# Optimization experiments

Measured on AMD Instinct MI355X. Metric: run time of the kernel, lower is better.

## Reference

```python
import jax, jax.numpy as jnp
import numpy as np

GROUP_SIZE = 128
EQN = "btd,kdf->btkf"  # x:[B,T,D] @ w:[K,D,F] -> [B,T,K,F]


def setup_inputs() -> dict:
    key = jax.random.key(0)
    k1, k2, k3, k4 = jax.random.split(key, 4)
    B, T, D = 4, 2048, 4096
    K, F = 2, 8192
    G = D // GROUP_SIZE  # 32 quantization groups along D
    x = jax.random.normal(k1, (B, T, D), dtype=jnp.float32)
    qweight = jax.random.randint(k2, (K, D, F), 0, 16, dtype=jnp.int32)  # uint4 values
    qzeros = jax.random.randint(k3, (K, G, F), 0, 16, dtype=jnp.int32)   # uint4 zero points
    scales = jax.random.uniform(k4, (K, G, F), dtype=jnp.float32) * 0.02
    return {"x": x, "qweight": qweight, "qzeros": qzeros, "scales": scales}


def dequantize(imatrix, scales, zeros, group_size, axis_to_repeat):
    rs = jnp.repeat(scales, group_size, axis=axis_to_repeat)
    rz = jnp.repeat(zeros, group_size, axis=axis_to_repeat)
    return (imatrix.astype(rs.dtype) - rz.astype(rs.dtype)) * rs


def reference(x, qweight, qzeros, scales):
    # dequantize int4 weights along axis 1 (hidden/contraction dim), then einsum
    w = dequantize(qweight, scales, qzeros, GROUP_SIZE, axis_to_repeat=1)  # [K,D,F] fp32
    w = w.astype(x.dtype)
    return jnp.einsum(EQN, x, w)  # [B,T,K,F]
```

## Files before the change

kernel.cpp:

```cpp
#include <hip/hip_runtime.h>
#include <hip/hip_bf16.h>
#include <stdint.h>


typedef __attribute__((ext_vector_type(8))) short bf16x8;
typedef __attribute__((ext_vector_type(16))) float f32x16;
typedef __attribute__((ext_vector_type(4))) float f32x4;

static constexpr int Dd = 4096, Ff = 8192;
static constexpr int M = 8192, NTOT = 16384;
static constexpr int NKT2 = Dd / 32;
static constexpr int NMB = M / 256;
static constexpr int NNB = NTOT / 256;

__device__ __forceinline__ short f2bf(float f) {
    __hip_bfloat16 h = __float2bfloat16(f);
    return *reinterpret_cast<short*>(&h);
}

__device__ __forceinline__ int frag_off32(int r, int cb) {
    const int rb = r >> 5, ks = cb >> 1, kh = cb & 1;
    return ((rb * 2 + ks) << 10) + (((r & 31) + 32 * kh) << 4);
}

__global__ __launch_bounds__(256) void xcvt(const float* __restrict__ x,
                                            char* __restrict__ Xw) {
    const int bid = blockIdx.x;
    const int h = bid >> 7, kt2 = bid & 127;
    const int t = threadIdx.x;
    const int r = t >> 1, seg = t & 1;
    const float* src = x + ((size_t)(h * 128 + r)) * Dd + kt2 * 32 + seg * 16;
    char* panel = Xw + ((size_t)bid << 13);
    #pragma unroll
    for (int jj = 0; jj < 2; ++jj) {
        float4 v0 = *reinterpret_cast<const float4*>(src + jj * 8);
        float4 v1 = *reinterpret_cast<const float4*>(src + jj * 8 + 4);
        union { short s[8]; bf16x8 v; } u;
        u.s[0] = f2bf(v0.x); u.s[1] = f2bf(v0.y); u.s[2] = f2bf(v0.z); u.s[3] = f2bf(v0.w);
        u.s[4] = f2bf(v1.x); u.s[5] = f2bf(v1.y); u.s[6] = f2bf(v1.z); u.s[7] = f2bf(v1.w);
        const int cb = seg * 2 + jj;
        *reinterpret_cast<bf16x8*>(panel + frag_off32(r, cb)) = u.v;
    }
}

__global__ __launch_bounds__(256) void wdq(const int* __restrict__ qw,
                                           const int* __restrict__ qz,
                                           const float* __restrict__ sc,
                                           char* __restrict__ Ww) {
    const int bid = blockIdx.x;
    const int fh = bid >> 7, kt2 = bid & 127;
    const int t = threadIdx.x;
    const int r = t & 127, dh = t >> 7;
    const int n = fh * 128 + r;
    const int k = n >> 13, f = n & 8191;
    const int g = kt2 >> 2;
    const int   zv = qz[((size_t)k * 32 + g) * Ff + f];
    const float sv = sc[((size_t)k * 32 + g) * Ff + f];
    const int* qp = qw + ((size_t)(k * Dd + kt2 * 32 + dh * 16)) * Ff + f;
    char* panel = Ww + ((size_t)bid << 13);
    #pragma unroll
    for (int jj = 0; jj < 2; ++jj) {
        union { short s[8]; bf16x8 v; } u;
        #pragma unroll
        for (int e = 0; e < 8; ++e) {
            int q = qp[(size_t)(jj * 8 + e) * Ff];
            u.s[e] = f2bf((float)(q - zv) * sv);
        }
        const int cb = dh * 2 + jj;
        *reinterpret_cast<bf16x8*>(panel + frag_off32(r, cb)) = u.v;
    }
}

#define APAN32(H, KT2) (Xw + (((size_t)(H) * 128 + (KT2)) << 13))
#define BPAN32(H, KT2) (Ww + (((size_t)(H) * 128 + (KT2)) << 13))

#define GLL(GP, LP)                                                                \
    __builtin_amdgcn_global_load_lds(                                              \
        (const __attribute__((address_space(1))) void*)(GP),                       \
        (__attribute__((address_space(3))) void*)(LP), 16, 0, 0)

#define STAGE_TILE(KT2, BUF) do {                                                  \
    GLL(APAN32(bm2,     (KT2)) + woff16, (BUF) +     0 + woffu);                   \
    GLL(APAN32(bm2 + 1, (KT2)) + woff16, (BUF) +  8192 + woffu);                   \
    GLL(BPAN32(bn2,     (KT2)) + woff16, (BUF) + 16384 + woffu);                   \
    GLL(BPAN32(bn2 + 1, (KT2)) + woff16, (BUF) + 24576 + woffu);                   \
} while (0)

#define SB0() __builtin_amdgcn_sched_barrier(0)

#define BODY(KT2, BUFR, DOST, BUFS) do {                                           \
    if (DOST) STAGE_TILE((KT2) + 2, BUFS);                                         \
    bf16x8 a[8], b[4];                                                             \
    _Pragma("unroll")                                                              \
    for (int mb = 0; mb < 4; ++mb)                                                 \
        _Pragma("unroll")                                                          \
        for (int ks = 0; ks < 2; ++ks)                                             \
            a[mb * 2 + ks] = *reinterpret_cast<const bf16x8*>(                     \
                (BUFR) + aoff + (mb * 2 + ks) * 1024);                             \
    _Pragma("unroll")                                                              \
    for (int nf = 0; nf < 2; ++nf)                                                 \
        _Pragma("unroll")                                                          \
        for (int ks = 0; ks < 2; ++ks)                                             \
            b[nf * 2 + ks] = *reinterpret_cast<const bf16x8*>(                     \
                (BUFR) + boff + nf * 2048 + ks * 1024);                            \
    _Pragma("unroll")                                                              \
    for (int ks = 0; ks < 2; ++ks)                                                 \
        _Pragma("unroll")                                                          \
        for (int mb = 0; mb < 4; ++mb)                                             \
            _Pragma("unroll")                                                      \
            for (int nf = 0; nf < 2; ++nf)                                         \
                acc[mb * 2 + nf] = __builtin_amdgcn_mfma_f32_32x32x16_bf16(        \
                    a[mb * 2 + ks], b[nf * 2 + ks], acc[mb * 2 + nf], 0, 0, 0);    \
    if (DOST) asm volatile("s_waitcnt vmcnt(4)" ::: "memory");                     \
    else      asm volatile("s_waitcnt vmcnt(0)" ::: "memory");                     \
    SB0();                                                                         \
    __builtin_amdgcn_s_barrier();                                                  \
    SB0();                                                                         \
} while (0)

__global__ __launch_bounds__(512, 2) void gemm256(const char* __restrict__ Xw,
                                                  const char* __restrict__ Ww,
                                                  float* __restrict__ out) {
    __shared__ char lds[131072];
    char* const L0 = lds;
    char* const L1 = lds + 32768;
    char* const L2 = lds + 65536;
    char* const L3 = lds + 98304;

    const int t = threadIdx.x;
    const int wave = t >> 6, lane = t & 63;
    const int wm = wave >> 2, wn = wave & 3;
    const int l31 = lane & 31;
    const int lane16 = lane << 4;

    const int xcd = blockIdx.x & 7;
    const int c   = blockIdx.x >> 3;
    const int bn  = xcd * 8 + (c >> 5);
    const int bm  = c & 31;
    const int bm2 = bm * 2, bn2 = bn * 2;

    const int woff16 = wave * 1024 + lane16;
    const int woffu  = wave * 1024;
    const int aoff = wm * 8192 + lane16;
    const int boff = 16384 + (wn >> 1) * 8192 + (wn & 1) * 4096 + lane16;

    f32x16 acc[8] = {};

    STAGE_TILE(0, L0);
    STAGE_TILE(1, L1);
    asm volatile("s_waitcnt vmcnt(4)" ::: "memory");
    SB0();
    __builtin_amdgcn_s_barrier();
    SB0();

    for (int i = 0; i < 32; ++i) {
        const int T = i * 4;
        const bool nl = (i < 31);
        BODY(T + 0, L0, true, L2);
        BODY(T + 1, L1, true, L3);
        BODY(T + 2, L2, nl,   L0);
        BODY(T + 3, L3, nl,   L1);
    }

    const int rbase = bm * 256 + wm * 128 + (lane >> 5) * 4;
    const int cbase = bn * 256 + wn * 64 + l31;
    #pragma unroll
    for (int mb = 0; mb < 4; ++mb)
        #pragma unroll
        for (int nf = 0; nf < 2; ++nf)
            #pragma unroll
            for (int reg = 0; reg < 16; ++reg) {
                const int row = rbase + mb * 32 + (reg & 3) + 8 * (reg >> 2);
                __builtin_nontemporal_store(
                    acc[mb * 2 + nf][reg],
                    &out[(size_t)row * NTOT + cbase + nf * 32]);
            }
}

#define LDP 72
__global__ __launch_bounds__(256) void int4_gemm(
    const float* __restrict__ x, const int* __restrict__ qw,
    const int* __restrict__ qz, const float* __restrict__ sc,
    float* __restrict__ out)
{
    __shared__ short As[128][LDP];
    __shared__ short Bs[128][LDP];
    const int t = threadIdx.x;
    int gid = (blockIdx.x & 7) * 1024 + (blockIdx.x >> 3);
    const int bm = gid & 63;
    const int bnq = gid >> 6;
    const int kse = bnq >> 6;
    const int f0  = (bnq & 63) * 128;
    const int m0  = bm * 128;
    const int wave = t >> 6, lane = t & 63;
    const int wm = wave >> 1, wn = wave & 1;
    const int l15 = lane & 15, lhi = lane >> 4;
    const int am = t >> 4, ad = (t & 15) * 4;
    const int bf = t & 127, bd = (t >> 7) * 4;
    const int*   qwk = qw + (size_t)kse * Dd * Ff;
    const int*   qzk = qz + (size_t)kse * 32 * Ff;
    const float* sck = sc + (size_t)kse * 32 * Ff;
    f32x4 acc[4][4] = {};
    for (int d0 = 0; d0 < Dd; d0 += 64) {
        __syncthreads();
        #pragma unroll
        for (int p = 0; p < 8; ++p) {
            int m = p * 16 + am;
            const float4 v = *reinterpret_cast<const float4*>(
                &x[(size_t)(m0 + m) * Dd + d0 + ad]);
            short4 wv;
            wv.x = f2bf(v.x); wv.y = f2bf(v.y); wv.z = f2bf(v.z); wv.w = f2bf(v.w);
            *reinterpret_cast<short4*>(&As[m][ad]) = wv;
        }
        {
            const int g = d0 >> 7;
            const int   zv = qzk[g * Ff + f0 + bf];
            const float sv = sck[g * Ff + f0 + bf];
            #pragma unroll
            for (int p = 0; p < 8; ++p) {
                int dl = p * 8 + bd;
                const int* qp = qwk + (size_t)(d0 + dl) * Ff + f0 + bf;
                short4 wv;
                wv.x = f2bf((float)(qp[0]      - zv) * sv);
                wv.y = f2bf((float)(qp[Ff]     - zv) * sv);
                wv.z = f2bf((float)(qp[2 * Ff] - zv) * sv);
                wv.w = f2bf((float)(qp[3 * Ff] - zv) * sv);
                *reinterpret_cast<short4*>(&Bs[bf][dl]) = wv;
            }
        }
        __syncthreads();
        #pragma unroll
        for (int kk = 0; kk < 64; kk += 32) {
            bf16x8 a2[4], b2[4];
            #pragma unroll
            for (int i = 0; i < 4; ++i)
                a2[i] = *reinterpret_cast<const bf16x8*>(&As[wm * 64 + i * 16 + l15][kk + lhi * 8]);
            #pragma unroll
            for (int i = 0; i < 4; ++i)
                b2[i] = *reinterpret_cast<const bf16x8*>(&Bs[wn * 64 + i * 16 + l15][kk + lhi * 8]);
            #pragma unroll
            for (int mi = 0; mi < 4; ++mi)
                #pragma unroll
                for (int ni = 0; ni < 4; ++ni)
                    acc[mi][ni] = __builtin_amdgcn_mfma_f32_16x16x32_bf16(
                        a2[mi], b2[ni], acc[mi][ni], 0, 0, 0);
        }
    }
    const int crow0 = m0 + wm * 64 + lhi * 4;
    const int ccol0 = bnq * 128 + wn * 64 + l15;
    #pragma unroll
    for (int mi = 0; mi < 4; ++mi)
        #pragma unroll
        for (int ni = 0; ni < 4; ++ni)
            #pragma unroll
            for (int r = 0; r < 4; ++r)
                out[(size_t)(crow0 + mi * 16 + r) * NTOT + ccol0 + ni * 16] =
                    acc[mi][ni][r];
}

extern "C" void kernel_launch(void* const* d_in, const int* in_sizes, int n_in,
                              void* d_out, int out_size, void* d_ws, size_t ws_size,
                              hipStream_t stream) {
    const float* x  = (const float*)d_in[0];
    const int*   qw = (const int*)d_in[1];
    const int*   qz = (const int*)d_in[2];
    const float* sc = (const float*)d_in[3];
    float*       out = (float*)d_out;

    const size_t xw_bytes = (size_t)(M / 128) * NKT2 * 8192;
    const size_t ww_bytes = (size_t)(NTOT / 128) * NKT2 * 8192;

    if (ws_size >= xw_bytes + ww_bytes) {
        char* Xw = (char*)d_ws;
        char* Ww = Xw + xw_bytes;
        hipLaunchKernelGGL(xcvt, dim3((M / 128) * NKT2), dim3(256), 0, stream, x, Xw);
        hipLaunchKernelGGL(wdq, dim3((NTOT / 128) * NKT2), dim3(256), 0, stream,
                           qw, qz, sc, Ww);
        hipLaunchKernelGGL(gemm256, dim3(NMB * NNB), dim3(512), 0, stream,
                           Xw, Ww, out);
    } else {
        hipLaunchKernelGGL(int4_gemm, dim3(8192), dim3(256), 0, stream,
                           x, qw, qz, sc, out);
    }
}
```

Before: 1.155 ms.

## Deepen LDS pipeline to three stages and double-buffer register fragments

The GEMM main loop now prefetches global tiles three steps ahead instead of two. It also loads the next tile's LDS fragments into a second register set while the MFMAs consume the current one, so LDS reads overlap with matrix math. MFMA sections are wrapped in s_setprio to favour this wave during compute. The change doubles the fragment registers, which may raise register pressure and affect occupancy at 2 blocks per CU.

```diff
diff --git a/kernel.cpp b/kernel.cpp
--- a/kernel.cpp
+++ b/kernel.cpp
@@ -88,21 +88,23 @@
 
 #define SB0() __builtin_amdgcn_sched_barrier(0)
 
-#define BODY(KT2, BUFR, DOST, BUFS) do {                                           \
-    if (DOST) STAGE_TILE((KT2) + 2, BUFS);                                         \
-    bf16x8 a[8], b[4];                                                             \
+#define READ12(BUF, A_, B_) do {                                                   \
     _Pragma("unroll")                                                              \
     for (int mb = 0; mb < 4; ++mb)                                                 \
         _Pragma("unroll")                                                          \
         for (int ks = 0; ks < 2; ++ks)                                             \
-            a[mb * 2 + ks] = *reinterpret_cast<const bf16x8*>(                     \
-                (BUFR) + aoff + (mb * 2 + ks) * 1024);                             \
+            A_[mb * 2 + ks] = *reinterpret_cast<const bf16x8*>(                    \
+                (BUF) + aoff + (mb * 2 + ks) * 1024);                              \
     _Pragma("unroll")                                                              \
     for (int nf = 0; nf < 2; ++nf)                                                 \
         _Pragma("unroll")                                                          \
         for (int ks = 0; ks < 2; ++ks)                                             \
-            b[nf * 2 + ks] = *reinterpret_cast<const bf16x8*>(                     \
-                (BUFR) + boff + nf * 2048 + ks * 1024);                            \
+            B_[nf * 2 + ks] = *reinterpret_cast<const bf16x8*>(                    \
+                (BUF) + boff + nf * 2048 + ks * 1024);                             \
+} while (0)
+
+#define MM16(A_, B_) do {                                                          \
+    __builtin_amdgcn_s_setprio(1);                                                 \
     _Pragma("unroll")                                                              \
     for (int ks = 0; ks < 2; ++ks)                                                 \
         _Pragma("unroll")                                                          \
@@ -110,7 +112,15 @@
             _Pragma("unroll")                                                      \
             for (int nf = 0; nf < 2; ++nf)                                         \
                 acc[mb * 2 + nf] = __builtin_amdgcn_mfma_f32_32x32x16_bf16(        \
-                    a[mb * 2 + ks], b[nf * 2 + ks], acc[mb * 2 + nf], 0, 0, 0);    \
+                    A_[mb * 2 + ks], B_[nf * 2 + ks], acc[mb * 2 + nf], 0, 0, 0);  \
+    __builtin_amdgcn_s_setprio(0);                                                 \
+} while (0)
+
+#define BODY(KT2, BUFN, BUFS, DOST, DORD, AS, BS, AD, BD) do {                     \
+    if (DOST) STAGE_TILE((KT2) + 3, BUFS);                                         \
+    if (DORD) READ12(BUFN, AD, BD);                                                \
+    SB0();                                                                         \
+    MM16(AS, BS);                                                                  \
     if (DOST) asm volatile("s_waitcnt vmcnt(4)" ::: "memory");                     \
     else      asm volatile("s_waitcnt vmcnt(0)" ::: "memory");                     \
     SB0();                                                                         \
@@ -144,22 +154,25 @@
     const int aoff = wm * 8192 + lane16;
     const int boff = 16384 + (wn >> 1) * 8192 + (wn & 1) * 4096 + lane16;
 
+    bf16x8 aP[8], bP[4], aQ[8], bQ[4];
     f32x16 acc[8] = {};
 
     STAGE_TILE(0, L0);
     STAGE_TILE(1, L1);
-    asm volatile("s_waitcnt vmcnt(4)" ::: "memory");
+    asm volatile("s_waitcnt vmcnt(0)" ::: "memory");
+    STAGE_TILE(2, L2);
     SB0();
     __builtin_amdgcn_s_barrier();
     SB0();
+    READ12(L0, aP, bP);
 
     for (int i = 0; i < 32; ++i) {
         const int T = i * 4;
-        const bool nl = (i < 31);
-        BODY(T + 0, L0, true, L2);
-        BODY(T + 1, L1, true, L3);
-        BODY(T + 2, L2, nl,   L0);
-        BODY(T + 3, L3, nl,   L1);
+        const bool full = (i < 31);
+        BODY(T + 0, L1, L3, true, true, aP, bP, aQ, bQ);
+        BODY(T + 1, L2, L0, full, true, aQ, bQ, aP, bP);
+        BODY(T + 2, L3, L1, full, true, aP, bP, aQ, bQ);
+        BODY(T + 3, L0, L2, full, full, aQ, bQ, aP, bP);
     }
 
     const int rbase = bm * 256 + wm * 128 + (lane >> 5) * 4;
```

Measured after the change: 1.189 ms. 1.03x slower.

## Load A fragments directly to registers and stage only B through LDS

Applied to the files above, without the earlier changes.

The A operand is now read from global memory straight into double-buffered register fragments (each wave reads its own rows), and only the B panel is staged through LDS with a 4-deep ring. This halves LDS usage and removes the LDS round trip for A. MFMA blocks are also wrapped in s_setprio to favour the math waves. The cost is higher VGPR pressure from the two A register sets, and per-wave global loads for A that other waves no longer share through LDS, which may limit occupancy or stall on memory latency.

```diff
diff --git a/kernel.cpp b/kernel.cpp
--- a/kernel.cpp
+++ b/kernel.cpp
@@ -79,30 +79,31 @@
         (const __attribute__((address_space(1))) void*)(GP),                       \
         (__attribute__((address_space(3))) void*)(LP), 16, 0, 0)
 
-#define STAGE_TILE(KT2, BUF) do {                                                  \
-    GLL(APAN32(bm2,     (KT2)) + woff16, (BUF) +     0 + woffu);                   \
-    GLL(APAN32(bm2 + 1, (KT2)) + woff16, (BUF) +  8192 + woffu);                   \
-    GLL(BPAN32(bn2,     (KT2)) + woff16, (BUF) + 16384 + woffu);                   \
-    GLL(BPAN32(bn2 + 1, (KT2)) + woff16, (BUF) + 24576 + woffu);                   \
-} while (0)
-
-#define SB0() __builtin_amdgcn_sched_barrier(0)
-
-#define BODY(KT2, BUFR, DOST, BUFS) do {                                           \
-    if (DOST) STAGE_TILE((KT2) + 2, BUFS);                                         \
-    bf16x8 a[8], b[4];                                                             \
+#define STAGEB(KT2, BUF) do {                                                      \
+    GLL(BPAN32(bn2,     (KT2)) + woff16, (BUF) + woffu);                           \
+    GLL(BPAN32(bn2 + 1, (KT2)) + woff16, (BUF) + 8192 + woffu);                    \
+} while (0)
+
+#define LOADA(KT2, DST) do {                                                       \
+    const char* _ap = APAN32(bm2 + wm, (KT2));                                     \
     _Pragma("unroll")                                                              \
-    for (int mb = 0; mb < 4; ++mb)                                                 \
-        _Pragma("unroll")                                                          \
-        for (int ks = 0; ks < 2; ++ks)                                             \
-            a[mb * 2 + ks] = *reinterpret_cast<const bf16x8*>(                     \
-                (BUFR) + aoff + (mb * 2 + ks) * 1024);                             \
+    for (int j = 0; j < 8; ++j)                                                    \
+        DST[j] = *reinterpret_cast<const bf16x8*>(_ap + (j << 10) + lane16);       \
+} while (0)
+
+#define READB(BUF) do {                                                            \
     _Pragma("unroll")                                                              \
     for (int nf = 0; nf < 2; ++nf)                                                 \
         _Pragma("unroll")                                                          \
         for (int ks = 0; ks < 2; ++ks)                                             \
-            b[nf * 2 + ks] = *reinterpret_cast<const bf16x8*>(                     \
-                (BUFR) + boff + nf * 2048 + ks * 1024);                            \
+            bbT[nf * 2 + ks] = *reinterpret_cast<const bf16x8*>(                   \
+                (BUF) + bsel + (((bnf2 + nf) * 2 + ks) << 10) + lane16);           \
+} while (0)
+
+#define SB0() __builtin_amdgcn_sched_barrier(0)
+
+#define MM16(A_) do {                                                              \
+    __builtin_amdgcn_s_setprio(1);                                                 \
     _Pragma("unroll")                                                              \
     for (int ks = 0; ks < 2; ++ks)                                                 \
         _Pragma("unroll")                                                          \
@@ -110,9 +111,21 @@
             _Pragma("unroll")                                                      \
             for (int nf = 0; nf < 2; ++nf)                                         \
                 acc[mb * 2 + nf] = __builtin_amdgcn_mfma_f32_32x32x16_bf16(        \
-                    a[mb * 2 + ks], b[nf * 2 + ks], acc[mb * 2 + nf], 0, 0, 0);    \
-    if (DOST) asm volatile("s_waitcnt vmcnt(4)" ::: "memory");                     \
-    else      asm volatile("s_waitcnt vmcnt(0)" ::: "memory");                     \
+                    A_[mb * 2 + ks], bbT[nf * 2 + ks], acc[mb * 2 + nf], 0, 0, 0); \
+    __builtin_amdgcn_s_setprio(0);                                                 \
+} while (0)
+
+#define VM10 asm volatile("s_waitcnt vmcnt(10)" ::: "memory")
+#define VM8  asm volatile("s_waitcnt vmcnt(8)"  ::: "memory")
+#define VM0  asm volatile("s_waitcnt vmcnt(0)"  ::: "memory")
+
+#define BODY(KT2, BUFB, ACUR, ANXT, DOLA, DOST, BUFS, VMW) do {                    \
+    if (DOLA) LOADA((KT2) + 1, ANXT);                                              \
+    if (DOST) STAGEB((KT2) + 3, BUFS);                                             \
+    READB(BUFB);                                                                   \
+    SB0();                                                                         \
+    MM16(ACUR);                                                                    \
+    VMW;                                                                           \
     SB0();                                                                         \
     __builtin_amdgcn_s_barrier();                                                  \
     SB0();                                                                         \
@@ -121,16 +134,15 @@
 __global__ __launch_bounds__(512, 2) void gemm256(const char* __restrict__ Xw,
                                                   const char* __restrict__ Ww,
                                                   float* __restrict__ out) {
-    __shared__ char lds[131072];
-    char* const L0 = lds;
-    char* const L1 = lds + 32768;
-    char* const L2 = lds + 65536;
-    char* const L3 = lds + 98304;
+    __shared__ char lds[65536];
+    char* const Lb0 = lds;
+    char* const Lb1 = lds + 16384;
+    char* const Lb2 = lds + 32768;
+    char* const Lb3 = lds + 49152;
 
     const int t = threadIdx.x;
     const int wave = t >> 6, lane = t & 63;
     const int wm = wave >> 2, wn = wave & 3;
-    const int l31 = lane & 31;
     const int lane16 = lane << 4;
 
     const int xcd = blockIdx.x & 7;
@@ -141,27 +153,36 @@
 
     const int woff16 = wave * 1024 + lane16;
     const int woffu  = wave * 1024;
-    const int aoff = wm * 8192 + lane16;
-    const int boff = 16384 + (wn >> 1) * 8192 + (wn & 1) * 4096 + lane16;
-
+    const int bsel = (wn >> 1) * 8192;
+    const int bnf2 = (wn & 1) * 2;
+
+    bf16x8 aP[8], aQ[8], bbT[4];
     f32x16 acc[8] = {};
 
-    STAGE_TILE(0, L0);
-    STAGE_TILE(1, L1);
-    asm volatile("s_waitcnt vmcnt(4)" ::: "memory");
+    STAGEB(0, Lb0);
+    STAGEB(1, Lb1);
+    STAGEB(2, Lb2);
+    SB0();
+    LOADA(0, aP);
+    SB0();
+    asm volatile("s_waitcnt vmcnt(8)" ::: "memory");
     SB0();
     __builtin_amdgcn_s_barrier();
     SB0();
 
-    for (int i = 0; i < 32; ++i) {
+    for (int i = 0; i < 31; ++i) {
         const int T = i * 4;
-        const bool nl = (i < 31);
-        BODY(T + 0, L0, true, L2);
-        BODY(T + 1, L1, true, L3);
-        BODY(T + 2, L2, nl,   L0);
-        BODY(T + 3, L3, nl,   L1);
-    }
-
+        BODY(T + 0, Lb0, aP, aQ, true, true, Lb3, VM10);
+        BODY(T + 1, Lb1, aQ, aP, true, true, Lb0, VM10);
+        BODY(T + 2, Lb2, aP, aQ, true, true, Lb1, VM10);
+        BODY(T + 3, Lb3, aQ, aP, true, true, Lb2, VM10);
+    }
+    BODY(124, Lb0, aP, aQ, true,  true,  Lb3, VM10);
+    BODY(125, Lb1, aQ, aP, true,  false, Lb0, VM10);
+    BODY(126, Lb2, aP, aQ, true,  false, Lb0, VM8);
+    BODY(127, Lb3, aQ, aP, false, false, Lb0, VM0);
+
+    const int l31 = lane & 31;
     const int rbase = bm * 256 + wm * 128 + (lane >> 5) * 4;
     const int cbase = bn * 256 + wn * 64 + l31;
     #pragma unroll
```

Result: slower. 1.483 ms (+28.3%).

## Load B fragments directly to registers and halve LDS with four-phase pipeline

Applied to the files above, without the earlier changes.

The GEMM main loop is restructured so only the A tile is staged through LDS, now double-buffered at 64 KiB instead of four 32 KiB buffers. B fragments are loaded straight from global memory into registers, ping-ponging between two register sets. Each 64-wide K step is split into four phases with barriers, and MFMA blocks are raised with s_setprio. This cuts LDS traffic and footprint for B and tries to overlap global loads with MFMA. In exchange it uses more registers, adds more barriers per iteration, and leans on global-load latency being hidden by the register prefetch.

```diff
diff --git a/kernel.cpp b/kernel.cpp
--- a/kernel.cpp
+++ b/kernel.cpp
@@ -79,58 +79,94 @@
         (const __attribute__((address_space(1))) void*)(GP),                       \
         (__attribute__((address_space(3))) void*)(LP), 16, 0, 0)
 
-#define STAGE_TILE(KT2, BUF) do {                                                  \
-    GLL(APAN32(bm2,     (KT2)) + woff16, (BUF) +     0 + woffu);                   \
-    GLL(APAN32(bm2 + 1, (KT2)) + woff16, (BUF) +  8192 + woffu);                   \
-    GLL(BPAN32(bn2,     (KT2)) + woff16, (BUF) + 16384 + woffu);                   \
-    GLL(BPAN32(bn2 + 1, (KT2)) + woff16, (BUF) + 24576 + woffu);                   \
-} while (0)
-
-#define SB0() __builtin_amdgcn_sched_barrier(0)
-
-#define BODY(KT2, BUFR, DOST, BUFS) do {                                           \
-    if (DOST) STAGE_TILE((KT2) + 2, BUFS);                                         \
-    bf16x8 a[8], b[4];                                                             \
-    _Pragma("unroll")                                                              \
-    for (int mb = 0; mb < 4; ++mb)                                                 \
-        _Pragma("unroll")                                                          \
-        for (int ks = 0; ks < 2; ++ks)                                             \
-            a[mb * 2 + ks] = *reinterpret_cast<const bf16x8*>(                     \
-                (BUFR) + aoff + (mb * 2 + ks) * 1024);                             \
+#define GLLA(KT64, MH, SUB, BUF)                                                   \
+    GLL(APAN32(bm2 + (MH), 2 * (KT64) + (SUB)) + woff16,                           \
+        (BUF) + (MH) * 16384 + (SUB) * 8192 + woffu)
+
+#define LOADB4(DST, KT64, KP) do {                                                 \
+    const char* _bp = BPAN32(bn2 + (wn >> 1), 2 * (KT64) + (KP));                  \
     _Pragma("unroll")                                                              \
     for (int nf = 0; nf < 2; ++nf)                                                 \
         _Pragma("unroll")                                                          \
-        for (int ks = 0; ks < 2; ++ks)                                             \
-            b[nf * 2 + ks] = *reinterpret_cast<const bf16x8*>(                     \
-                (BUFR) + boff + nf * 2048 + ks * 1024);                            \
+        for (int kq = 0; kq < 2; ++kq)                                             \
+            DST[nf * 2 + kq] = *reinterpret_cast<const bf16x8*>(                   \
+                _bp + (((bnf2 + nf) * 2 + kq) << 10) + lane16);                    \
+} while (0)
+
+#define RDA4(LA, H, KP) do {                                                       \
     _Pragma("unroll")                                                              \
-    for (int ks = 0; ks < 2; ++ks)                                                 \
+    for (int mf = 0; mf < 2; ++mf)                                                 \
         _Pragma("unroll")                                                          \
-        for (int mb = 0; mb < 4; ++mb)                                             \
+        for (int kq = 0; kq < 2; ++kq)                                             \
+            af[mf * 2 + kq] = *reinterpret_cast<const bf16x8*>(                    \
+                (LA) + wm * 16384 + (KP) * 8192 +                                  \
+                ((((H) * 2 + mf) * 2 + kq) << 10) + lane16);                       \
+} while (0)
+
+#define SB0() __builtin_amdgcn_sched_barrier(0)
+#define PHW() do {                                                                 \
+    SB0();                                                                         \
+    __builtin_amdgcn_s_barrier();                                                  \
+    asm volatile("s_waitcnt lgkmcnt(0)" ::: "memory");                             \
+    SB0();                                                                         \
+} while (0)
+#define PHE() do { SB0(); __builtin_amdgcn_s_barrier(); } while (0)
+
+#define MM8(H, BB) do {                                                            \
+    __builtin_amdgcn_s_setprio(1);                                                 \
+    _Pragma("unroll")                                                              \
+    for (int kq = 0; kq < 2; ++kq)                                                 \
+        _Pragma("unroll")                                                          \
+        for (int mf = 0; mf < 2; ++mf)                                             \
             _Pragma("unroll")                                                      \
             for (int nf = 0; nf < 2; ++nf)                                         \
-                acc[mb * 2 + nf] = __builtin_amdgcn_mfma_f32_32x32x16_bf16(        \
-                    a[mb * 2 + ks], b[nf * 2 + ks], acc[mb * 2 + nf], 0, 0, 0);    \
-    if (DOST) asm volatile("s_waitcnt vmcnt(4)" ::: "memory");                     \
-    else      asm volatile("s_waitcnt vmcnt(0)" ::: "memory");                     \
-    SB0();                                                                         \
-    __builtin_amdgcn_s_barrier();                                                  \
-    SB0();                                                                         \
+                acc[((H) * 2 + mf) * 2 + nf] = __builtin_amdgcn_mfma_f32_32x32x16_bf16( \
+                    af[mf * 2 + kq], BB[nf * 2 + kq],                              \
+                    acc[((H) * 2 + mf) * 2 + nf], 0, 0, 0);                        \
+    __builtin_amdgcn_s_setprio(0);                                                 \
+} while (0)
+
+#define VM4 asm volatile("s_waitcnt vmcnt(4)" ::: "memory")
+#define VM0 asm volatile("s_waitcnt vmcnt(0)" ::: "memory")
+
+#define BODY4(U, LAc, LAn, DOST, DOB3, VMW) do {                                   \
+                                 \
+    LOADB4(bbY, (U), 1);                                                           \
+    RDA4(LAc, 0, 0);                                                               \
+    PHW();                                                                         \
+    MM8(0, bbX);                                                                   \
+    PHE();                                                                         \
+                                                         \
+    if (DOST) { GLLA((U) + 1, 0, 0, LAn); GLLA((U) + 1, 0, 1, LAn); }              \
+    RDA4(LAc, 1, 0);                                                               \
+    PHW();                                                                         \
+    MM8(1, bbX);                                                                   \
+    PHE();                                                                         \
+                                \
+    if (DOST) { GLLA((U) + 1, 1, 0, LAn); GLLA((U) + 1, 1, 1, LAn); }              \
+    if (DOB3) LOADB4(bbX, (U) + 1, 0);                                             \
+    RDA4(LAc, 0, 1);                                                               \
+    PHW();                                                                         \
+    MM8(0, bbY);                                                                   \
+    PHE();                                                                         \
+                            \
+    RDA4(LAc, 1, 1);                                                               \
+    PHW();                                                                         \
+    MM8(1, bbY);                                                                   \
+    VMW;                                                                           \
+    PHE();                                                                         \
 } while (0)
 
 __global__ __launch_bounds__(512, 2) void gemm256(const char* __restrict__ Xw,
                                                   const char* __restrict__ Ww,
                                                   float* __restrict__ out) {
-    __shared__ char lds[131072];
-    char* const L0 = lds;
-    char* const L1 = lds + 32768;
-    char* const L2 = lds + 65536;
-    char* const L3 = lds + 98304;
+    __shared__ char lds[65536];
+    char* const lA0 = lds;
+    char* const lA1 = lds + 32768;
 
     const int t = threadIdx.x;
     const int wave = t >> 6, lane = t & 63;
     const int wm = wave >> 2, wn = wave & 3;
-    const int l31 = lane & 31;
     const int lane16 = lane << 4;
 
     const int xcd = blockIdx.x & 7;
@@ -141,27 +177,28 @@
 
     const int woff16 = wave * 1024 + lane16;
     const int woffu  = wave * 1024;
-    const int aoff = wm * 8192 + lane16;
-    const int boff = 16384 + (wn >> 1) * 8192 + (wn & 1) * 4096 + lane16;
-
+    const int bnf2 = (wn & 1) * 2;
+
+    bf16x8 af[4], bbX[4], bbY[4];
     f32x16 acc[8] = {};
 
-    STAGE_TILE(0, L0);
-    STAGE_TILE(1, L1);
-    asm volatile("s_waitcnt vmcnt(4)" ::: "memory");
+    GLLA(0, 0, 0, lA0); GLLA(0, 0, 1, lA0);
+    GLLA(0, 1, 0, lA0); GLLA(0, 1, 1, lA0);
+    LOADB4(bbX, 0, 0);
+    VM4;
     SB0();
     __builtin_amdgcn_s_barrier();
     SB0();
 
     for (int i = 0; i < 32; ++i) {
-        const int T = i * 4;
+        const int U = 2 * i;
         const bool nl = (i < 31);
-        BODY(T + 0, L0, true, L2);
-        BODY(T + 1, L1, true, L3);
-        BODY(T + 2, L2, nl,   L0);
-        BODY(T + 3, L3, nl,   L1);
-    }
-
+        BODY4(U,     lA0, lA1, true, true, VM4);
+        if (nl) { BODY4(U + 1, lA1, lA0, true, true, VM4); }
+        else    { BODY4(U + 1, lA1, lA0, false, false, VM0); }
+    }
+
+    const int l31 = lane & 31;
     const int rbase = bm * 256 + wm * 128 + (lane >> 5) * 4;
     const int cbase = bn * 256 + wn * 64 + l31;
     #pragma unroll
```

Result: slower. 1.487 ms (+28.7%).
